# Kernel optimization log

Measured on AMD Instinct MI355X. Metric: run time of the kernel, lower is better.

## Reference

```python
import jax, jax.numpy as jnp
import numpy as np

B, T, N_EMBD, HEAD = 1024, 256, 384, 64


def setup_inputs() -> dict:
    key = jax.random.key(0)
    kx, kq, kk, kv = jax.random.split(key, 4)
    x = jax.random.normal(kx, (B, T, N_EMBD), dtype=jnp.float32)
    # torch nn.Linear(384, 64, bias=False) weight is [64, 384]; we store the
    # transposed [384, 64] form so forward is x @ W.
    s = 1.0 / np.sqrt(N_EMBD)
    Wq = jax.random.normal(kq, (N_EMBD, HEAD), dtype=jnp.float32) * s
    Wk = jax.random.normal(kk, (N_EMBD, HEAD), dtype=jnp.float32) * s
    Wv = jax.random.normal(kv, (N_EMBD, HEAD), dtype=jnp.float32) * s
    return {"x": x, "Wq": Wq, "Wk": Wk, "Wv": Wv}


def reference(x, Wq, Wk, Wv):
    # Single-head causal self-attention (eval mode: dropout is identity).
    q = jnp.einsum('btn,nh->bth', x, Wq)  # [B,T,H]
    k = jnp.einsum('btn,nh->bth', x, Wk)
    v = jnp.einsum('btn,nh->bth', x, Wv)
    scale = 1.0 / jnp.sqrt(jnp.asarray(HEAD, dtype=x.dtype))
    wei = jnp.einsum('bth,bsh->bts', q, k) * scale  # [B,T,T]
    causal = jnp.tril(jnp.ones((T, T), dtype=bool))
    wei = jnp.where(causal[None, :, :], wei, -jnp.inf)
    wei = jax.nn.softmax(wei, axis=-1)
    out = jnp.einsum('bts,bsh->bth', wei, v)  # [B,T,H]
    return out
```

## Files before the change

kernel.cpp:

```cpp
#include <hip/hip_runtime.h>

#define BB 1024
#define TT 256
#define EE 384
#define HH 64

typedef float  f32x4  __attribute__((ext_vector_type(4)));
typedef short  short8 __attribute__((ext_vector_type(8)));
typedef unsigned short us4 __attribute__((ext_vector_type(4)));

__device__ __forceinline__ unsigned short f2bf(float f) {
    unsigned int u = __float_as_uint(f);
    u += 0x7FFFu + ((u >> 16) & 1u);
    return (unsigned short)(u >> 16);
}

__device__ __forceinline__ void gl_lds16(const void* g, void* l) {
    __builtin_amdgcn_global_load_lds(
        (const __attribute__((address_space(1))) unsigned int*)g,
        (__attribute__((address_space(3))) unsigned int*)l, 16, 0, 0);
}


__global__ void prep2_kernel(const float* __restrict__ Wq, const float* __restrict__ Wk,
                             const float* __restrict__ Wv, unsigned short* __restrict__ Wt2) {
    int i = blockIdx.x * 256 + threadIdx.x;
    if (i >= 12 * 6144) return;
    int kt = i / 6144;
    int r1 = i - kt * 6144;
    int n  = r1 >> 5;
    int r2 = r1 & 31;
    int sc = r2 >> 3, e = r2 & 7;
    int c  = sc ^ (n & 3);
    int k  = kt * 32 + c * 8 + e;
    float v;
    if (n < 64)       v = Wq[k * HH + n] * 0.18033688011112042f;
    else if (n < 128) v = Wk[k * HH + (n - 64)];
    else              v = Wv[k * HH + (n - 128)];
    Wt2[i] = f2bf(v);
}

__global__ __launch_bounds__(256, 2) void qkv_kernel(const float* __restrict__ x,
                                                     const unsigned short* __restrict__ Wt2,
                                                     unsigned short* __restrict__ Qimg,
                                                     unsigned short* __restrict__ Kimg,
                                                     unsigned short* __restrict__ Vimg) {
    __shared__ __align__(16) float          xs[128 * 32];
    __shared__ __align__(16) unsigned short wts[6144];

    const int tid  = threadIdx.x;
    const int lane = tid & 63;
    const int w    = tid >> 6;
    const int g    = lane >> 4;
    const int mr   = lane & 15;
    const int m7   = mr & 7;
    const int m3   = mr & 3;
    const long rows0 = (long)blockIdx.x * 128;

    f32x4 acc[2][12];
#pragma unroll
    for (int ti = 0; ti < 2; ++ti)
#pragma unroll
        for (int nt = 0; nt < 12; ++nt) acc[ti][nt] = (f32x4){0.f, 0.f, 0.f, 0.f};

    const int swb = (g ^ m3) << 3;

    for (int kt = 0; kt < 12; ++kt) {
        __syncthreads();
#pragma unroll
        for (int j = 0; j < 4; ++j) {
            int chunk = j * 256 + tid;
            int r = chunk >> 3, c = chunk & 7;
            const float* src = x + (rows0 + r) * EE + kt * 32 + ((c ^ (r & 7)) << 2);
            gl_lds16(src, xs + (j * 256 + w * 64) * 4);
        }
#pragma unroll
        for (int j = 0; j < 3; ++j) {
            int ch = j * 256 + tid;
            gl_lds16(Wt2 + kt * 6144 + ch * 8, wts + (j * 256 + w * 64) * 8);
        }
        __syncthreads();

        short8 afr[2];
#pragma unroll
        for (int ti = 0; ti < 2; ++ti) {
            const int lr = w * 32 + ti * 16 + mr;
            const float* base = xs + lr * 32;
            f32x4 lo = *(const f32x4*)(base + (((2 * g)     ^ m7) << 2));
            f32x4 hi = *(const f32x4*)(base + (((2 * g + 1) ^ m7) << 2));
            union { short8 v; unsigned short u[8]; } cv;
            cv.u[0] = f2bf(lo.x); cv.u[1] = f2bf(lo.y); cv.u[2] = f2bf(lo.z); cv.u[3] = f2bf(lo.w);
            cv.u[4] = f2bf(hi.x); cv.u[5] = f2bf(hi.y); cv.u[6] = f2bf(hi.z); cv.u[7] = f2bf(hi.w);
            afr[ti] = cv.v;
        }
#pragma unroll
        for (int nt = 0; nt < 12; ++nt) {
            short8 bfr = *(const short8*)(wts + (nt * 16 + mr) * 32 + swb);
            acc[0][nt] = __builtin_amdgcn_mfma_f32_16x16x32_bf16(afr[0], bfr, acc[0][nt], 0, 0, 0);
            acc[1][nt] = __builtin_amdgcn_mfma_f32_16x16x32_bf16(afr[1], bfr, acc[1][nt], 0, 0, 0);
        }
    }

    const int b  = blockIdx.x >> 1;
    const int t0 = (blockIdx.x & 1) * 128;
    unsigned short* Qb = Qimg + (size_t)b * 16384;
    unsigned short* Kb = Kimg + (size_t)b * 16384;
    unsigned short* Vb = Vimg + (size_t)b * 16384;

#pragma unroll
    for (int ti = 0; ti < 2; ++ti) {
        const int tbase = t0 + w * 32 + ti * 16;
#pragma unroll
        for (int nt = 0; nt < 12; ++nt) {
            f32x4 v = acc[ti][nt];
            if (nt < 4) {
                const int h = nt * 16 + mr;
#pragma unroll
                for (int r = 0; r < 4; ++r)
                    Qb[(tbase + g * 4 + r) * 64 + h] = f2bf(v[r]);
            } else if (nt < 8) {
                const int hc = (nt - 4) * 2 + (mr >> 3);
#pragma unroll
                for (int r = 0; r < 4; ++r) {
                    const int t = tbase + g * 4 + r;
                    Kb[t * 64 + ((hc ^ (t & 7)) << 3) + m7] = f2bf(v[r]);
                }
            } else {
                const int h  = (nt - 8) * 16 + mr;
                const int tq = tbase + g * 4;
                const int sw = (tq >> 3) ^ m7;
                us4 pk;
                pk.x = f2bf(v[0]); pk.y = f2bf(v[1]); pk.z = f2bf(v[2]); pk.w = f2bf(v[3]);
                *(us4*)(Vb + h * 256 + sw * 8 + (tq & 7)) = pk;
            }
        }
    }
}

__global__ __launch_bounds__(512, 4) void attn2_kernel(const unsigned short* __restrict__ Qimg,
                                                       const unsigned short* __restrict__ Kimg,
                                                       const unsigned short* __restrict__ Vimg,
                                                       float* __restrict__ out) {
    __shared__ __align__(16) unsigned short Ks[16384];
    __shared__ __align__(16) unsigned short Vs[16384];
    __shared__ __align__(16) unsigned short Ps[8192];

    const int tid  = threadIdx.x;
    const int lane = tid & 63;
    const int w    = tid >> 6;
    const int g    = lane >> 4;
    const int mr   = lane & 15;
    const int m7   = mr & 7;
    const int b    = blockIdx.x;

    const unsigned short* Qb = Qimg + (size_t)b * 16384;
    const unsigned short* Kb = Kimg + (size_t)b * 16384;
    const unsigned short* Vb = Vimg + (size_t)b * 16384;

    short8 qfr[2][2];
#pragma unroll
    for (int p = 0; p < 2; ++p) {
        const int t0 = (w + p * 8) * 16;
#pragma unroll
        for (int kt = 0; kt < 2; ++kt)
            qfr[p][kt] = *(const short8*)(Qb + (t0 + mr) * 64 + kt * 32 + g * 8);
    }

#pragma unroll
    for (int j = 0; j < 4; ++j) {
        int ch = j * 512 + tid;
        gl_lds16(Kb + ch * 8, Ks + (j * 512 + w * 64) * 8);
    }
#pragma unroll
    for (int j = 0; j < 4; ++j) {
        int ch = j * 512 + tid;
        gl_lds16(Vb + ch * 8, Vs + (j * 512 + w * 64) * 8);
    }
    __syncthreads();

    const int swv0 = ((0 * 4 + g) ^ m7) << 3;
    const int swv1 = ((1 * 4 + g) ^ m7) << 3;
    unsigned short* pw = Ps + w * 1024;

    short8 ones;
#pragma unroll
    for (int i = 0; i < 8; ++i) ones[i] = (short)0x3F80;

#pragma unroll
    for (int p = 0; p < 2; ++p) {
        const int a   = w + p * 8;
        const int r0  = a * 16;
        const int nch = (a >> 2) + 1;

        f32x4 o[4];
        f32x4 ls = (f32x4){0.f, 0.f, 0.f, 0.f};
        float mrun[4];
#pragma unroll
        for (int i = 0; i < 4; ++i) { o[i] = (f32x4){0.f, 0.f, 0.f, 0.f}; mrun[i] = -3.0e38f; }

        for (int j = 0; j < nch; ++j) {
            f32x4 s[4];
#pragma unroll
            for (int nt = 0; nt < 4; ++nt) s[nt] = (f32x4){0.f, 0.f, 0.f, 0.f};
#pragma unroll
            for (int kt = 0; kt < 2; ++kt) {
                const short8 qf = qfr[p][kt];
                const int swv = kt ? swv1 : swv0;
#pragma unroll
                for (int nt = 0; nt < 4; ++nt) {
                    short8 kf = *(const short8*)(Ks + (j * 64 + nt * 16 + mr) * 64 + swv);
                    s[nt] = __builtin_amdgcn_mfma_f32_16x16x32_bf16(qf, kf, s[nt], 0, 0, 0);
                }
            }
            if (j == nch - 1) {
#pragma unroll
                for (int nt = 0; nt < 4; ++nt) {
                    const int key = j * 64 + nt * 16 + mr;
#pragma unroll
                    for (int r = 0; r < 4; ++r)
                        if (key > r0 + g * 4 + r) s[nt][r] = -3.0e38f;
                }
            }
            float cm[4], al[4];
#pragma unroll
            for (int r = 0; r < 4; ++r) {
                cm[r] = fmaxf(fmaxf(s[0][r], s[1][r]), fmaxf(s[2][r], s[3][r]));
                cm[r] = fmaxf(cm[r], __shfl_xor(cm[r], 1, 64));
                cm[r] = fmaxf(cm[r], __shfl_xor(cm[r], 2, 64));
                cm[r] = fmaxf(cm[r], __shfl_xor(cm[r], 4, 64));
                cm[r] = fmaxf(cm[r], __shfl_xor(cm[r], 8, 64));
                float mn = fmaxf(mrun[r], cm[r]);
                al[r] = exp2f(mrun[r] - mn);
                mrun[r] = mn;
            }
#pragma unroll
            for (int nt = 0; nt < 4; ++nt) {
#pragma unroll
                for (int r = 0; r < 4; ++r) {
                    const int lr = g * 4 + r;
                    const int sw = (nt * 2 + (mr >> 3)) ^ (lr & 7);
                    pw[lr * 64 + (sw << 3) + m7] = f2bf(exp2f(s[nt][r] - mrun[r]));
                }
            }
#pragma unroll
            for (int hn = 0; hn < 4; ++hn)
#pragma unroll
                for (int r = 0; r < 4; ++r) o[hn][r] *= al[r];
#pragma unroll
            for (int r = 0; r < 4; ++r) ls[r] *= al[r];
#pragma unroll
            for (int kt = 0; kt < 2; ++kt) {
                const int swv = kt ? swv1 : swv0;
                short8 pf = *(const short8*)(pw + mr * 64 + swv);
#pragma unroll
                for (int hn = 0; hn < 4; ++hn) {
                    short8 vf = *(const short8*)(Vs + (hn * 16 + mr) * 256 + j * 64 + swv);
                    o[hn] = __builtin_amdgcn_mfma_f32_16x16x32_bf16(pf, vf, o[hn], 0, 0, 0);
                }
                ls = __builtin_amdgcn_mfma_f32_16x16x32_bf16(pf, ones, ls, 0, 0, 0);
            }
        }
        float* ob = out + ((size_t)b * TT + r0) * HH;
#pragma unroll
        for (int r = 0; r < 4; ++r) {
            const float inv = 1.0f / ls[r];
#pragma unroll
            for (int hn = 0; hn < 4; ++hn)
                ob[(g * 4 + r) * HH + hn * 16 + mr] = o[hn][r] * inv;
        }
    }
}


__global__ void prep_kernel(const float* __restrict__ Wq, const float* __restrict__ Wk,
                            const float* __restrict__ Wv, unsigned short* __restrict__ Wt) {
    int i = blockIdx.x * 256 + threadIdx.x;
    if (i >= 192 * EE) return;
    int n = i / EE, k = i - n * EE;
    float v;
    if (n < 64)       v = Wq[k * HH + n] * 0.18033688011112042f;
    else if (n < 128) v = Wk[k * HH + (n - 64)];
    else              v = Wv[k * HH + (n - 128)];
    Wt[i] = f2bf(v);
}

__global__ __launch_bounds__(512, 2) void attn_kernel(const float* __restrict__ x,
                                                      const unsigned short* __restrict__ Wt,
                                                      float* __restrict__ out) {
    __shared__ unsigned short Qs[TT * 72];
    __shared__ unsigned short Ksh[TT * 72];
    __shared__ unsigned short Vt[HH * 264];
    __shared__ unsigned short Psc[8 * 1152];

    const int tid  = threadIdx.x;
    const int lane = tid & 63;
    const int w    = tid >> 6;
    const int g    = lane >> 4;
    const int mr   = lane & 15;
    const int b    = blockIdx.x;
    const float* xb = x + (size_t)b * (TT * EE);

    f32x4 acc[2][12];
#pragma unroll
    for (int ti = 0; ti < 2; ++ti)
#pragma unroll
        for (int nt = 0; nt < 12; ++nt) acc[ti][nt] = (f32x4){0.f, 0.f, 0.f, 0.f};

    const int M0a = (2 * w) * 16, M0b = (2 * w + 1) * 16;

    for (int kt = 0; kt < 12; ++kt) {
        const int k0 = kt * 32 + g * 8;
        short8 bfr[12];
#pragma unroll
        for (int nt = 0; nt < 12; ++nt)
            bfr[nt] = *(const short8*)(Wt + (size_t)(nt * 16 + mr) * EE + k0);
        short8 afr[2];
#pragma unroll
        for (int ti = 0; ti < 2; ++ti) {
            const int m0 = ti ? M0b : M0a;
            const float* ap = xb + (size_t)(m0 + mr) * EE + k0;
            f32x4 lo = *(const f32x4*)ap;
            f32x4 hi = *(const f32x4*)(ap + 4);
            union { short8 v; unsigned short u[8]; } cv;
            cv.u[0] = f2bf(lo.x); cv.u[1] = f2bf(lo.y); cv.u[2] = f2bf(lo.z); cv.u[3] = f2bf(lo.w);
            cv.u[4] = f2bf(hi.x); cv.u[5] = f2bf(hi.y); cv.u[6] = f2bf(hi.z); cv.u[7] = f2bf(hi.w);
            afr[ti] = cv.v;
        }
#pragma unroll
        for (int nt = 0; nt < 12; ++nt) {
            acc[0][nt] = __builtin_amdgcn_mfma_f32_16x16x32_bf16(afr[0], bfr[nt], acc[0][nt], 0, 0, 0);
            acc[1][nt] = __builtin_amdgcn_mfma_f32_16x16x32_bf16(afr[1], bfr[nt], acc[1][nt], 0, 0, 0);
        }
    }

#pragma unroll
    for (int ti = 0; ti < 2; ++ti) {
        const int row = (ti ? M0b : M0a) + g * 4;
#pragma unroll
        for (int nt = 0; nt < 12; ++nt) {
            f32x4 v = acc[ti][nt];
            if (nt < 4) {
                const int col = nt * 16 + mr;
#pragma unroll
                for (int r = 0; r < 4; ++r) Qs[(row + r) * 72 + col] = f2bf(v[r]);
            } else if (nt < 8) {
                const int col = (nt - 4) * 16 + mr;
#pragma unroll
                for (int r = 0; r < 4; ++r) Ksh[(row + r) * 72 + col] = f2bf(v[r]);
            } else {
                const int h = (nt - 8) * 16 + mr;
                us4 pk;
                pk.x = f2bf(v[0]); pk.y = f2bf(v[1]); pk.z = f2bf(v[2]); pk.w = f2bf(v[3]);
                *(us4*)(&Vt[h * 264 + row]) = pk;
            }
        }
    }
    __syncthreads();

#pragma unroll
    for (int pass = 0; pass < 2; ++pass) {
        const int a  = pass ? (15 - w) : w;
        const int r0 = a * 16;
        f32x4 o[4];
        float mrun[4], lrun[4];
#pragma unroll
        for (int i = 0; i < 4; ++i) {
            o[i] = (f32x4){0.f, 0.f, 0.f, 0.f};
            mrun[i] = -3.0e38f; lrun[i] = 0.f;
        }
        const int nch = (a >> 2) + 1;
        unsigned short* pwv = Psc + w * 1152;

        for (int j = 0; j < nch; ++j) {
            f32x4 s[4];
#pragma unroll
            for (int nt = 0; nt < 4; ++nt) s[nt] = (f32x4){0.f, 0.f, 0.f, 0.f};
#pragma unroll
            for (int kt = 0; kt < 2; ++kt) {
                short8 qf = *(const short8*)(Qs + (r0 + mr) * 72 + kt * 32 + g * 8);
#pragma unroll
                for (int nt = 0; nt < 4; ++nt) {
                    short8 kf = *(const short8*)(Ksh + (j * 64 + nt * 16 + mr) * 72 + kt * 32 + g * 8);
                    s[nt] = __builtin_amdgcn_mfma_f32_16x16x32_bf16(qf, kf, s[nt], 0, 0, 0);
                }
            }
            if (j * 64 + 63 > r0) {
#pragma unroll
                for (int nt = 0; nt < 4; ++nt) {
                    const int key = j * 64 + nt * 16 + mr;
#pragma unroll
                    for (int r = 0; r < 4; ++r)
                        if (key > r0 + g * 4 + r) s[nt][r] = -3.0e38f;
                }
            }
            float cm[4];
#pragma unroll
            for (int r = 0; r < 4; ++r) {
                cm[r] = fmaxf(fmaxf(s[0][r], s[1][r]), fmaxf(s[2][r], s[3][r]));
                cm[r] = fmaxf(cm[r], __shfl_xor(cm[r], 1, 64));
                cm[r] = fmaxf(cm[r], __shfl_xor(cm[r], 2, 64));
                cm[r] = fmaxf(cm[r], __shfl_xor(cm[r], 4, 64));
                cm[r] = fmaxf(cm[r], __shfl_xor(cm[r], 8, 64));
            }
            float al[4];
#pragma unroll
            for (int r = 0; r < 4; ++r) {
                float mn = fmaxf(mrun[r], cm[r]);
                al[r] = exp2f(mrun[r] - mn);
                mrun[r] = mn;
            }
            float rs[4] = {0.f, 0.f, 0.f, 0.f};
#pragma unroll
            for (int nt = 0; nt < 4; ++nt) {
#pragma unroll
                for (int r = 0; r < 4; ++r) {
                    float pv = exp2f(s[nt][r] - mrun[r]);
                    rs[r] += pv;
                    pwv[(g * 4 + r) * 72 + nt * 16 + mr] = f2bf(pv);
                }
            }
#pragma unroll
            for (int r = 0; r < 4; ++r) {
                rs[r] += __shfl_xor(rs[r], 1, 64);
                rs[r] += __shfl_xor(rs[r], 2, 64);
                rs[r] += __shfl_xor(rs[r], 4, 64);
                rs[r] += __shfl_xor(rs[r], 8, 64);
                lrun[r] = lrun[r] * al[r] + rs[r];
            }
#pragma unroll
            for (int hn = 0; hn < 4; ++hn)
#pragma unroll
                for (int r = 0; r < 4; ++r) o[hn][r] *= al[r];
#pragma unroll
            for (int kt = 0; kt < 2; ++kt) {
                short8 pf = *(const short8*)(pwv + mr * 72 + kt * 32 + g * 8);
#pragma unroll
                for (int hn = 0; hn < 4; ++hn) {
                    short8 vf = *(const short8*)(Vt + (hn * 16 + mr) * 264 + j * 64 + kt * 32 + g * 8);
                    o[hn] = __builtin_amdgcn_mfma_f32_16x16x32_bf16(pf, vf, o[hn], 0, 0, 0);
                }
            }
        }
        float* ob = out + ((size_t)b * TT + r0) * HH;
#pragma unroll
        for (int r = 0; r < 4; ++r) {
            const float inv = 1.0f / lrun[r];
#pragma unroll
            for (int hn = 0; hn < 4; ++hn)
                ob[(g * 4 + r) * HH + hn * 16 + mr] = o[hn][r] * inv;
        }
    }
}


extern "C" void kernel_launch(void* const* d_in, const int* in_sizes, int n_in,
                              void* d_out, int out_size, void* d_ws, size_t ws_size,
                              hipStream_t stream) {
    const float* x  = (const float*)d_in[0];
    const float* Wq = (const float*)d_in[1];
    const float* Wk = (const float*)d_in[2];
    const float* Wv = (const float*)d_in[3];
    float* out = (float*)d_out;

    const size_t img = (size_t)1024 * 16384;
    const size_t need = 147456 + 3 * img * 2;

    if (ws_size >= need) {
        unsigned short* Wt2  = (unsigned short*)d_ws;
        unsigned short* Qimg = (unsigned short*)((char*)d_ws + 147456);
        unsigned short* Kimg = Qimg + img;
        unsigned short* Vimg = Kimg + img;
        prep2_kernel<<<288, 256, 0, stream>>>(Wq, Wk, Wv, Wt2);
        qkv_kernel<<<2048, 256, 0, stream>>>(x, Wt2, Qimg, Kimg, Vimg);
        attn2_kernel<<<1024, 512, 0, stream>>>(Qimg, Kimg, Vimg, out);
    } else {
        unsigned short* Wt = (unsigned short*)d_ws;
        prep_kernel<<<288, 256, 0, stream>>>(Wq, Wk, Wv, Wt);
        attn_kernel<<<BB, 512, 0, stream>>>(x, Wt, out);
    }
}
```

Baseline: 605.3 us.

## Fuse QKV projection and attention into one kernel keeping K/V in LDS

Merges the QKV projection and the attention kernel into one per-batch kernel with 512 threads. Q, K and V are written straight into shared memory instead of going to global workspace images and being read back, which removes roughly 100MB of intermediate bf16 traffic and one launch. Each wave now handles query tiles w and 15-w so the causal work is balanced. In exchange the projection runs with a single 256-row block per batch, occupancy is capped at 2 blocks per CU, and LDS is reused across phases, which needs careful synchronization.

```diff
diff --git a/kernel.cpp b/kernel.cpp
--- a/kernel.cpp
+++ b/kernel.cpp
@@ -20,7 +20,6 @@
         (const __attribute__((address_space(1))) unsigned int*)g,
         (__attribute__((address_space(3))) unsigned int*)l, 16, 0, 0);
 }
-
 
 __global__ void prep2_kernel(const float* __restrict__ Wq, const float* __restrict__ Wk,
                              const float* __restrict__ Wv, unsigned short* __restrict__ Wt2) {
@@ -40,13 +39,15 @@
     Wt2[i] = f2bf(v);
 }
 
-__global__ __launch_bounds__(256, 2) void qkv_kernel(const float* __restrict__ x,
-                                                     const unsigned short* __restrict__ Wt2,
-                                                     unsigned short* __restrict__ Qimg,
-                                                     unsigned short* __restrict__ Kimg,
-                                                     unsigned short* __restrict__ Vimg) {
-    __shared__ __align__(16) float          xs[128 * 32];
-    __shared__ __align__(16) unsigned short wts[6144];
+__global__ __launch_bounds__(512, 2) void fused_kernel(const float* __restrict__ x,
+                                                       const unsigned short* __restrict__ Wt2,
+                                                       float* __restrict__ out) {
+    __shared__ __align__(16) unsigned short Ks[16384];
+    __shared__ __align__(16) unsigned short Vs[16384];
+    __shared__ __align__(16) unsigned short Ps[8192];
+
+    float*          xs  = (float*)Ks;
+    unsigned short* wts = Vs;
 
     const int tid  = threadIdx.x;
     const int lane = tid & 63;
@@ -55,7 +56,8 @@
     const int mr   = lane & 15;
     const int m7   = mr & 7;
     const int m3   = mr & 3;
-    const long rows0 = (long)blockIdx.x * 128;
+    const int b    = blockIdx.x;
+    const float* xb = x + (size_t)b * TT * EE;
 
     f32x4 acc[2][12];
 #pragma unroll
@@ -63,28 +65,31 @@
 #pragma unroll
         for (int nt = 0; nt < 12; ++nt) acc[ti][nt] = (f32x4){0.f, 0.f, 0.f, 0.f};
 
-    const int swb = (g ^ m3) << 3;
+    const int swb   = (g ^ m3) << 3;
+    const int tileA = w;
+    const int tileB = 15 - w;
 
     for (int kt = 0; kt < 12; ++kt) {
+#pragma unroll
+        for (int j = 0; j < 4; ++j) {
+            int chunk = j * 512 + tid;
+            int r = chunk >> 3, c = chunk & 7;
+            const float* src = xb + r * EE + kt * 32 + ((c ^ (r & 7)) << 2);
+            gl_lds16(src, xs + (j * 512 + w * 64) * 4);
+        }
+        {
+            gl_lds16(Wt2 + kt * 6144 + tid * 8, wts + (w * 64) * 8);
+        }
+        if (tid < 256) {
+            int ch = 512 + tid;
+            gl_lds16(Wt2 + kt * 6144 + ch * 8, wts + (512 + w * 64) * 8);
+        }
         __syncthreads();
-#pragma unroll
-        for (int j = 0; j < 4; ++j) {
-            int chunk = j * 256 + tid;
-            int r = chunk >> 3, c = chunk & 7;
-            const float* src = x + (rows0 + r) * EE + kt * 32 + ((c ^ (r & 7)) << 2);
-            gl_lds16(src, xs + (j * 256 + w * 64) * 4);
-        }
-#pragma unroll
-        for (int j = 0; j < 3; ++j) {
-            int ch = j * 256 + tid;
-            gl_lds16(Wt2 + kt * 6144 + ch * 8, wts + (j * 256 + w * 64) * 8);
-        }
-        __syncthreads();
 
         short8 afr[2];
 #pragma unroll
         for (int ti = 0; ti < 2; ++ti) {
-            const int lr = w * 32 + ti * 16 + mr;
+            const int lr = (ti ? tileB : tileA) * 16 + mr;
             const float* base = xs + lr * 32;
             f32x4 lo = *(const f32x4*)(base + (((2 * g)     ^ m7) << 2));
             f32x4 hi = *(const f32x4*)(base + (((2 * g + 1) ^ m7) << 2));
@@ -99,88 +104,56 @@
             acc[0][nt] = __builtin_amdgcn_mfma_f32_16x16x32_bf16(afr[0], bfr, acc[0][nt], 0, 0, 0);
             acc[1][nt] = __builtin_amdgcn_mfma_f32_16x16x32_bf16(afr[1], bfr, acc[1][nt], 0, 0, 0);
         }
-    }
-
-    const int b  = blockIdx.x >> 1;
-    const int t0 = (blockIdx.x & 1) * 128;
-    unsigned short* Qb = Qimg + (size_t)b * 16384;
-    unsigned short* Kb = Kimg + (size_t)b * 16384;
-    unsigned short* Vb = Vimg + (size_t)b * 16384;
+        __syncthreads();
+    }
 
 #pragma unroll
     for (int ti = 0; ti < 2; ++ti) {
-        const int tbase = t0 + w * 32 + ti * 16;
-#pragma unroll
-        for (int nt = 0; nt < 12; ++nt) {
+        const int tbase = (ti ? tileB : tileA) * 16;
+#pragma unroll
+        for (int nt = 4; nt < 8; ++nt) {
+            const int hc = (nt - 4) * 2 + (mr >> 3);
             f32x4 v = acc[ti][nt];
-            if (nt < 4) {
-                const int h = nt * 16 + mr;
-#pragma unroll
-                for (int r = 0; r < 4; ++r)
-                    Qb[(tbase + g * 4 + r) * 64 + h] = f2bf(v[r]);
-            } else if (nt < 8) {
-                const int hc = (nt - 4) * 2 + (mr >> 3);
-#pragma unroll
-                for (int r = 0; r < 4; ++r) {
-                    const int t = tbase + g * 4 + r;
-                    Kb[t * 64 + ((hc ^ (t & 7)) << 3) + m7] = f2bf(v[r]);
-                }
-            } else {
-                const int h  = (nt - 8) * 16 + mr;
-                const int tq = tbase + g * 4;
-                const int sw = (tq >> 3) ^ m7;
-                us4 pk;
-                pk.x = f2bf(v[0]); pk.y = f2bf(v[1]); pk.z = f2bf(v[2]); pk.w = f2bf(v[3]);
-                *(us4*)(Vb + h * 256 + sw * 8 + (tq & 7)) = pk;
-            }
-        }
-    }
-}
-
-__global__ __launch_bounds__(512, 4) void attn2_kernel(const unsigned short* __restrict__ Qimg,
-                                                       const unsigned short* __restrict__ Kimg,
-                                                       const unsigned short* __restrict__ Vimg,
-                                                       float* __restrict__ out) {
-    __shared__ __align__(16) unsigned short Ks[16384];
-    __shared__ __align__(16) unsigned short Vs[16384];
-    __shared__ __align__(16) unsigned short Ps[8192];
-
-    const int tid  = threadIdx.x;
-    const int lane = tid & 63;
-    const int w    = tid >> 6;
-    const int g    = lane >> 4;
-    const int mr   = lane & 15;
-    const int m7   = mr & 7;
-    const int b    = blockIdx.x;
-
-    const unsigned short* Qb = Qimg + (size_t)b * 16384;
-    const unsigned short* Kb = Kimg + (size_t)b * 16384;
-    const unsigned short* Vb = Vimg + (size_t)b * 16384;
-
+#pragma unroll
+            for (int r = 0; r < 4; ++r) {
+                const int t = tbase + g * 4 + r;
+                Ks[t * 64 + ((hc ^ (t & 7)) << 3) + m7] = f2bf(v[r]);
+            }
+        }
+#pragma unroll
+        for (int nt = 8; nt < 12; ++nt) {
+            const int h  = (nt - 8) * 16 + mr;
+            const int tq = tbase + g * 4;
+            const int sw = (tq >> 3) ^ m7;
+            f32x4 v = acc[ti][nt];
+            us4 pk;
+            pk.x = f2bf(v[0]); pk.y = f2bf(v[1]); pk.z = f2bf(v[2]); pk.w = f2bf(v[3]);
+            *(us4*)(Vs + h * 256 + sw * 8 + (tq & 7)) = pk;
+        }
+    }
+
+    unsigned short* pw = Ps + w * 1024;
     short8 qfr[2][2];
 #pragma unroll
     for (int p = 0; p < 2; ++p) {
-        const int t0 = (w + p * 8) * 16;
+#pragma unroll
+        for (int nt = 0; nt < 4; ++nt) {
+            f32x4 v = acc[p][nt];
+#pragma unroll
+            for (int r = 0; r < 4; ++r) {
+                const int lr = g * 4 + r;
+                const int sw = (nt * 2 + (mr >> 3)) ^ (lr & 7);
+                pw[lr * 64 + (sw << 3) + m7] = f2bf(v[r]);
+            }
+        }
 #pragma unroll
         for (int kt = 0; kt < 2; ++kt)
-            qfr[p][kt] = *(const short8*)(Qb + (t0 + mr) * 64 + kt * 32 + g * 8);
-    }
-
-#pragma unroll
-    for (int j = 0; j < 4; ++j) {
-        int ch = j * 512 + tid;
-        gl_lds16(Kb + ch * 8, Ks + (j * 512 + w * 64) * 8);
-    }
-#pragma unroll
-    for (int j = 0; j < 4; ++j) {
-        int ch = j * 512 + tid;
-        gl_lds16(Vb + ch * 8, Vs + (j * 512 + w * 64) * 8);
+            qfr[p][kt] = *(const short8*)(pw + mr * 64 + (((kt * 4 + g) ^ m7) << 3));
     }
     __syncthreads();
 
     const int swv0 = ((0 * 4 + g) ^ m7) << 3;
     const int swv1 = ((1 * 4 + g) ^ m7) << 3;
-    unsigned short* pw = Ps + w * 1024;
 
     short8 ones;
 #pragma unroll
@@ -188,7 +161,7 @@
 
 #pragma unroll
     for (int p = 0; p < 2; ++p) {
-        const int a   = w + p * 8;
+        const int a   = p ? (15 - w) : w;
         const int r0  = a * 16;
         const int nch = (a >> 2) + 1;
 
@@ -272,187 +245,6 @@
 }
 
 
-__global__ void prep_kernel(const float* __restrict__ Wq, const float* __restrict__ Wk,
-                            const float* __restrict__ Wv, unsigned short* __restrict__ Wt) {
-    int i = blockIdx.x * 256 + threadIdx.x;
-    if (i >= 192 * EE) return;
-    int n = i / EE, k = i - n * EE;
-    float v;
-    if (n < 64)       v = Wq[k * HH + n] * 0.18033688011112042f;
-    else if (n < 128) v = Wk[k * HH + (n - 64)];
-    else              v = Wv[k * HH + (n - 128)];
-    Wt[i] = f2bf(v);
-}
-
-__global__ __launch_bounds__(512, 2) void attn_kernel(const float* __restrict__ x,
-                                                      const unsigned short* __restrict__ Wt,
-                                                      float* __restrict__ out) {
-    __shared__ unsigned short Qs[TT * 72];
-    __shared__ unsigned short Ksh[TT * 72];
-    __shared__ unsigned short Vt[HH * 264];
-    __shared__ unsigned short Psc[8 * 1152];
-
-    const int tid  = threadIdx.x;
-    const int lane = tid & 63;
-    const int w    = tid >> 6;
-    const int g    = lane >> 4;
-    const int mr   = lane & 15;
-    const int b    = blockIdx.x;
-    const float* xb = x + (size_t)b * (TT * EE);
-
-    f32x4 acc[2][12];
-#pragma unroll
-    for (int ti = 0; ti < 2; ++ti)
-#pragma unroll
-        for (int nt = 0; nt < 12; ++nt) acc[ti][nt] = (f32x4){0.f, 0.f, 0.f, 0.f};
-
-    const int M0a = (2 * w) * 16, M0b = (2 * w + 1) * 16;
-
-    for (int kt = 0; kt < 12; ++kt) {
-        const int k0 = kt * 32 + g * 8;
-        short8 bfr[12];
-#pragma unroll
-        for (int nt = 0; nt < 12; ++nt)
-            bfr[nt] = *(const short8*)(Wt + (size_t)(nt * 16 + mr) * EE + k0);
-        short8 afr[2];
-#pragma unroll
-        for (int ti = 0; ti < 2; ++ti) {
-            const int m0 = ti ? M0b : M0a;
-            const float* ap = xb + (size_t)(m0 + mr) * EE + k0;
-            f32x4 lo = *(const f32x4*)ap;
-            f32x4 hi = *(const f32x4*)(ap + 4);
-            union { short8 v; unsigned short u[8]; } cv;
-            cv.u[0] = f2bf(lo.x); cv.u[1] = f2bf(lo.y); cv.u[2] = f2bf(lo.z); cv.u[3] = f2bf(lo.w);
-            cv.u[4] = f2bf(hi.x); cv.u[5] = f2bf(hi.y); cv.u[6] = f2bf(hi.z); cv.u[7] = f2bf(hi.w);
-            afr[ti] = cv.v;
-        }
-#pragma unroll
-        for (int nt = 0; nt < 12; ++nt) {
-            acc[0][nt] = __builtin_amdgcn_mfma_f32_16x16x32_bf16(afr[0], bfr[nt], acc[0][nt], 0, 0, 0);
-            acc[1][nt] = __builtin_amdgcn_mfma_f32_16x16x32_bf16(afr[1], bfr[nt], acc[1][nt], 0, 0, 0);
-        }
-    }
-
-#pragma unroll
-    for (int ti = 0; ti < 2; ++ti) {
-        const int row = (ti ? M0b : M0a) + g * 4;
-#pragma unroll
-        for (int nt = 0; nt < 12; ++nt) {
-            f32x4 v = acc[ti][nt];
-            if (nt < 4) {
-                const int col = nt * 16 + mr;
-#pragma unroll
-                for (int r = 0; r < 4; ++r) Qs[(row + r) * 72 + col] = f2bf(v[r]);
-            } else if (nt < 8) {
-                const int col = (nt - 4) * 16 + mr;
-#pragma unroll
-                for (int r = 0; r < 4; ++r) Ksh[(row + r) * 72 + col] = f2bf(v[r]);
-            } else {
-                const int h = (nt - 8) * 16 + mr;
-                us4 pk;
-                pk.x = f2bf(v[0]); pk.y = f2bf(v[1]); pk.z = f2bf(v[2]); pk.w = f2bf(v[3]);
-                *(us4*)(&Vt[h * 264 + row]) = pk;
-            }
-        }
-    }
-    __syncthreads();
-
-#pragma unroll
-    for (int pass = 0; pass < 2; ++pass) {
-        const int a  = pass ? (15 - w) : w;
-        const int r0 = a * 16;
-        f32x4 o[4];
-        float mrun[4], lrun[4];
-#pragma unroll
-        for (int i = 0; i < 4; ++i) {
-            o[i] = (f32x4){0.f, 0.f, 0.f, 0.f};
-            mrun[i] = -3.0e38f; lrun[i] = 0.f;
-        }
-        const int nch = (a >> 2) + 1;
-        unsigned short* pwv = Psc + w * 1152;
-
-        for (int j = 0; j < nch; ++j) {
-            f32x4 s[4];
-#pragma unroll
-            for (int nt = 0; nt < 4; ++nt) s[nt] = (f32x4){0.f, 0.f, 0.f, 0.f};
-#pragma unroll
-            for (int kt = 0; kt < 2; ++kt) {
-                short8 qf = *(const short8*)(Qs + (r0 + mr) * 72 + kt * 32 + g * 8);
-#pragma unroll
-                for (int nt = 0; nt < 4; ++nt) {
-                    short8 kf = *(const short8*)(Ksh + (j * 64 + nt * 16 + mr) * 72 + kt * 32 + g * 8);
-                    s[nt] = __builtin_amdgcn_mfma_f32_16x16x32_bf16(qf, kf, s[nt], 0, 0, 0);
-                }
-            }
-            if (j * 64 + 63 > r0) {
-#pragma unroll
-                for (int nt = 0; nt < 4; ++nt) {
-                    const int key = j * 64 + nt * 16 + mr;
-#pragma unroll
-                    for (int r = 0; r < 4; ++r)
-                        if (key > r0 + g * 4 + r) s[nt][r] = -3.0e38f;
-                }
-            }
-            float cm[4];
-#pragma unroll
-            for (int r = 0; r < 4; ++r) {
-                cm[r] = fmaxf(fmaxf(s[0][r], s[1][r]), fmaxf(s[2][r], s[3][r]));
-                cm[r] = fmaxf(cm[r], __shfl_xor(cm[r], 1, 64));
-                cm[r] = fmaxf(cm[r], __shfl_xor(cm[r], 2, 64));
-                cm[r] = fmaxf(cm[r], __shfl_xor(cm[r], 4, 64));
-                cm[r] = fmaxf(cm[r], __shfl_xor(cm[r], 8, 64));
-            }
-            float al[4];
-#pragma unroll
-            for (int r = 0; r < 4; ++r) {
-                float mn = fmaxf(mrun[r], cm[r]);
-                al[r] = exp2f(mrun[r] - mn);
-                mrun[r] = mn;
-            }
-            float rs[4] = {0.f, 0.f, 0.f, 0.f};
-#pragma unroll
-            for (int nt = 0; nt < 4; ++nt) {
-#pragma unroll
-                for (int r = 0; r < 4; ++r) {
-                    float pv = exp2f(s[nt][r] - mrun[r]);
-                    rs[r] += pv;
-                    pwv[(g * 4 + r) * 72 + nt * 16 + mr] = f2bf(pv);
-                }
-            }
-#pragma unroll
-            for (int r = 0; r < 4; ++r) {
-                rs[r] += __shfl_xor(rs[r], 1, 64);
-                rs[r] += __shfl_xor(rs[r], 2, 64);
-                rs[r] += __shfl_xor(rs[r], 4, 64);
-                rs[r] += __shfl_xor(rs[r], 8, 64);
-                lrun[r] = lrun[r] * al[r] + rs[r];
-            }
-#pragma unroll
-            for (int hn = 0; hn < 4; ++hn)
-#pragma unroll
-                for (int r = 0; r < 4; ++r) o[hn][r] *= al[r];
-#pragma unroll
-            for (int kt = 0; kt < 2; ++kt) {
-                short8 pf = *(const short8*)(pwv + mr * 72 + kt * 32 + g * 8);
-#pragma unroll
-                for (int hn = 0; hn < 4; ++hn) {
-                    short8 vf = *(const short8*)(Vt + (hn * 16 + mr) * 264 + j * 64 + kt * 32 + g * 8);
-                    o[hn] = __builtin_amdgcn_mfma_f32_16x16x32_bf16(pf, vf, o[hn], 0, 0, 0);
-                }
-            }
-        }
-        float* ob = out + ((size_t)b * TT + r0) * HH;
-#pragma unroll
-        for (int r = 0; r < 4; ++r) {
-            const float inv = 1.0f / lrun[r];
-#pragma unroll
-            for (int hn = 0; hn < 4; ++hn)
-                ob[(g * 4 + r) * HH + hn * 16 + mr] = o[hn][r] * inv;
-        }
-    }
-}
-
-
 extern "C" void kernel_launch(void* const* d_in, const int* in_sizes, int n_in,
                               void* d_out, int out_size, void* d_ws, size_t ws_size,
                               hipStream_t stream) {
@@ -462,20 +254,7 @@
     const float* Wv = (const float*)d_in[3];
     float* out = (float*)d_out;
 
-    const size_t img = (size_t)1024 * 16384;
-    const size_t need = 147456 + 3 * img * 2;
-
-    if (ws_size >= need) {
-        unsigned short* Wt2  = (unsigned short*)d_ws;
-        unsigned short* Qimg = (unsigned short*)((char*)d_ws + 147456);
-        unsigned short* Kimg = Qimg + img;
-        unsigned short* Vimg = Kimg + img;
-        prep2_kernel<<<288, 256, 0, stream>>>(Wq, Wk, Wv, Wt2);
-        qkv_kernel<<<2048, 256, 0, stream>>>(x, Wt2, Qimg, Kimg, Vimg);
-        attn2_kernel<<<1024, 512, 0, stream>>>(Qimg, Kimg, Vimg, out);
-    } else {
-        unsigned short* Wt = (unsigned short*)d_ws;
-        prep_kernel<<<288, 256, 0, stream>>>(Wq, Wk, Wv, Wt);
-        attn_kernel<<<BB, 512, 0, stream>>>(x, Wt, out);
-    }
-}
+    unsigned short* Wt2 = (unsigned short*)d_ws;
+    prep2_kernel<<<288, 256, 0, stream>>>(Wq, Wk, Wv, Wt2);
+    fused_kernel<<<BB, 512, 0, stream>>>(x, Wt2, out);
+}
```

New measurement: 588.4 us. 1.03x faster.
